# Performance work log

Hardware: AMD Instinct MI355X
Metric: run time of the kernel (lower is better)

## Reference

```python
import jax, jax.numpy as jnp
import numpy as np

B, N, C, H, M, T, L = 2, 4096, 256, 8, 48, 10000, 256
CH = C // H
HID = 512  # mlp_ratio=2


def _ln(x, g, b, eps=1e-5):
    mu = x.mean(-1, keepdims=True)
    var = ((x - mu) ** 2).mean(-1, keepdims=True)
    return (x - mu) * jax.lax.rsqrt(var + eps) * g + b


def setup_inputs() -> dict:
    key = jax.random.key(0)
    ks = iter(jax.random.split(key, 40))
    nrm = lambda shape, s=0.02: jax.random.normal(next(ks), shape, jnp.float32) * s
    return dict(
        feat=jax.random.normal(next(ks), (B, N, C), jnp.float32),
        memory=jax.random.normal(next(ks), (B, L, C), jnp.float32),
        member_idx=jax.random.randint(next(ks), (B, N, M), 0, N),
        cluster_mask=jax.random.randint(next(ks), (B, N, M), 0, 2, jnp.int32),
        pe_idx=jax.random.randint(next(ks), (B, N, M), 0, T),
        global_attn=0,
        pre_table=jax.random.normal(next(ks), (T, 5), jnp.float32),
        Wq=nrm((C, C)), bq=jnp.zeros(C), Wkv=nrm((C, 2 * C)), bkv=jnp.zeros(2 * C),
        blank_k=nrm((C,), 1.0), blank_v=nrm((C,), 1.0),
        Wpe=nrm((5, H)), bpe=jnp.zeros(H),
        Wproj=nrm((C, C)), bproj=jnp.zeros(C),
        g1=jnp.ones(C), be1=jnp.zeros(C), g2=jnp.ones(C), be2=jnp.zeros(C),
        xWq=nrm((C, C)), xbq=jnp.zeros(C), xWk=nrm((C, C)), xbk=jnp.zeros(C),
        xWv=nrm((C, C)), xbv=jnp.zeros(C), xWo=nrm((C, C)), xbo=jnp.zeros(C),
        xg=jnp.ones(C), xbe=jnp.zeros(C),
        W1=nrm((C, HID)), bf1=jnp.zeros(HID), W2=nrm((HID, C)), bf2=jnp.zeros(C),
    )


def _cluster_attn(x, member_idx, cluster_mask, pe_idx, pre_table,
                  Wq, bq, Wkv, bkv, blank_k, blank_v, Wpe, bpe, Wproj, bproj):
    b, n, c = x.shape
    scale = CH ** -0.5
    q = ((x @ Wq + bq) * scale).reshape(b, n, H, CH).transpose(0, 2, 1, 3)  # bhnc
    kv = (x @ Wkv + bkv).reshape(b, n, H, 2, CH)
    k = kv[..., 0, :].transpose(0, 2, 1, 3)  # bhnc
    v = kv[..., 1, :].transpose(0, 2, 1, 3)  # bhnc
    # CLUSTENQK: gather per-token neighborhood keys, dot with q -> b h n m
    gather = jax.vmap(lambda t, idx: t[:, idx, :])  # (h,n,c),(n,m)->(h,n,m,c)
    k_g = gather(k, member_idx)
    attn = jnp.einsum('bhnc,bhnmc->bhnm', q, k_g)
    # positional embedding table lookup
    pe_table = pre_table @ Wpe + bpe                 # T x H
    pos = pe_table[pe_idx].transpose(0, 3, 1, 2)     # b h n m
    attn = attn + pos
    maskf = cluster_mask.astype(attn.dtype)[:, None]  # b 1 n m
    attn = attn + (1.0 - maskf) * -100.0
    blank_attn = jnp.einsum('bhnc,hc->bhn', q, blank_k.reshape(H, CH))[..., None]
    p = jax.nn.softmax(jnp.concatenate([attn, blank_attn], axis=-1), axis=-1)
    pa, pb = p[..., :-1], p[..., -1:]
    # CLUSTENAV: gather values, weighted sum
    v_g = gather(v, member_idx)
    out = jnp.einsum('bhnm,bhnmc->bhnc', pa, v_g)
    out = out + pb * blank_v.reshape(1, H, 1, CH)
    out = out.transpose(0, 2, 1, 3).reshape(b, n, c)
    return out @ Wproj + bproj


def _cross_attn(tgt, memory, xWq, xbq, xWk, xbk, xWv, xbv, xWo, xbo, xg, xbe):
    b, n, c = tgt.shape
    t2 = _ln(tgt, xg, xbe)  # normalize_before=True
    q = (t2 @ xWq + xbq).reshape(b, n, H, CH).transpose(0, 2, 1, 3) * (CH ** -0.5)
    k = (memory @ xWk + xbk).reshape(b, -1, H, CH).transpose(0, 2, 1, 3)
    v = (memory @ xWv + xbv).reshape(b, -1, H, CH).transpose(0, 2, 1, 3)
    p = jax.nn.softmax(jnp.einsum('bhnc,bhlc->bhnl', q, k), axis=-1)
    o = jnp.einsum('bhnl,bhlc->bhnc', p, v).transpose(0, 2, 1, 3).reshape(b, n, c)
    return tgt + (o @ xWo + xbo)


def reference(feat, memory, member_idx, cluster_mask, pe_idx, global_attn, pre_table,
              Wq, bq, Wkv, bkv, blank_k, blank_v, Wpe, bpe, Wproj, bproj,
              g1, be1, g2, be2,
              xWq, xbq, xWk, xbk, xWv, xbv, xWo, xbo, xg, xbe,
              W1, bf1, W2, bf2):
    # global_attn is a static flag; this reference covers the local-cluster path
    assert global_attn == 0
    # local cluster attention with pre-norm residual (drop_path/layer_scale disabled)
    feat = feat + _cluster_attn(_ln(feat, g1, be1), member_idx, cluster_mask, pe_idx,
                                pre_table, Wq, bq, Wkv, bkv, blank_k, blank_v,
                                Wpe, bpe, Wproj, bproj)
    # cross attention to memory (pre-norm, residual inside)
    feat = _cross_attn(feat, memory, xWq, xbq, xWk, xbk, xWv, xbv, xWo, xbo, xg, xbe)
    # MLP block
    h = jax.nn.gelu(_ln(feat, g2, be2) @ W1 + bf1, approximate=False)
    feat = feat + (h @ W2 + bf2)
    return feat
```

## Files before the change

kernel.cpp:

```cpp
#include <hip/hip_runtime.h>
#include <hip/hip_bf16.h>
#include <math.h>

#define BB 2
#define NN 4096
#define CC 256
#define HH 8
#define MM 48
#define TT 10000
#define LL 256
#define CHDIM 32
#define HIDD 512
#define ROWS (BB*NN)

typedef __attribute__((ext_vector_type(8))) short bf16x8;
typedef __attribute__((ext_vector_type(4))) float f32x4;

static __device__ __forceinline__ short f2bf(float x) {
    __hip_bfloat16 h = __float2bfloat16(x);
    return *reinterpret_cast<short*>(&h);
}
static __device__ __forceinline__ float bf2f(short s) {
    unsigned int u = ((unsigned int)(unsigned short)s) << 16;
    union { unsigned int u; float f; } c; c.u = u;
    return c.f;
}

struct WtDesc { const float* src; __hip_bfloat16* dst; int K; int N; int tile0; float scl; };
struct WtArgs { WtDesc d[9]; };

__global__ __launch_bounds__(256) void prep_all_kernel(WtArgs a,
    const float* __restrict__ pre, const float* __restrict__ Wpe,
    const float* __restrict__ bpe, float* __restrict__ pet,
    const float* __restrict__ bq, const float* __restrict__ bkv,
    const float* __restrict__ xbk, const float* __restrict__ xbv,
    const float* __restrict__ xbq, float scale,
    float* __restrict__ bqkv, float* __restrict__ xbkv, float* __restrict__ xbqS,
    const float* __restrict__ memory, __hip_bfloat16* __restrict__ memBf) {
    __shared__ float tile[32][33];
    int bid = blockIdx.x, tid = threadIdx.x;
    if (bid < 768) {
        int mi = 0;
        #pragma unroll
        for (int i = 1; i < 9; ++i) if (bid >= a.d[i].tile0) mi = i;
        WtDesc dsc = a.d[mi];
        int t = bid - dsc.tile0;
        int tiles_n = dsc.N >> 5;
        int k0 = (t / tiles_n) * 32, n0 = (t % tiles_n) * 32;
        int tx = tid & 31, ty = tid >> 5;
        #pragma unroll
        for (int i = 0; i < 32; i += 8)
            tile[ty + i][tx] = dsc.src[(size_t)(k0 + ty + i) * dsc.N + n0 + tx];
        __syncthreads();
        #pragma unroll
        for (int i = 0; i < 32; i += 8)
            dsc.dst[(size_t)(n0 + ty + i) * dsc.K + k0 + tx] = __float2bfloat16(tile[tx][ty + i] * dsc.scl);
        return;
    }
    bid -= 768;
    if (bid < 313) {
        int i = bid * 256 + tid;
        if (i >= TT * HH) return;
        int t = i / HH, h = i % HH;
        float s = bpe[h];
        #pragma unroll
        for (int j = 0; j < 5; ++j) s += pre[t * 5 + j] * Wpe[j * HH + h];
        pet[i] = s;
    } else if (bid < 319) {
        int i = (bid - 313) * 256 + tid;
        if (i < 256) bqkv[i] = bq[i] * scale;
        else if (i < 768) bqkv[i] = bkv[i - 256];
        else if (i < 1024) xbkv[i - 768] = xbk[i - 768];
        else if (i < 1280) xbkv[256 + i - 1024] = xbv[i - 1024];
        else if (i < 1536) xbqS[i - 1280] = xbq[i - 1280] * scale;
    } else {
        int i = (bid - 319) * 256 + tid;
        if (i < 131072) memBf[i] = __float2bfloat16(memory[i]);
    }
}

__global__ __launch_bounds__(256) void ln_kernel(const float* __restrict__ in,
                                                 const float* __restrict__ g,
                                                 const float* __restrict__ b,
                                                 __hip_bfloat16* __restrict__ out) {
    int wave = threadIdx.x >> 6, lane = threadIdx.x & 63;
    int row = blockIdx.x * 4 + wave;
    float4 v = ((const float4*)(in + (size_t)row * CC))[lane];
    float s = (v.x + v.y) + (v.z + v.w);
    #pragma unroll
    for (int off = 32; off; off >>= 1) s += __shfl_xor(s, off, 64);
    float mu = s * (1.0f / 256.0f);
    float dx = v.x - mu, dy = v.y - mu, dz = v.z - mu, dw = v.w - mu;
    float s2 = (dx * dx + dy * dy) + (dz * dz + dw * dw);
    #pragma unroll
    for (int off = 32; off; off >>= 1) s2 += __shfl_xor(s2, off, 64);
    float rs = rsqrtf(s2 * (1.0f / 256.0f) + 1e-5f);
    float4 g4 = ((const float4*)g)[lane];
    float4 b4 = ((const float4*)b)[lane];
    ushort4 o4;
    o4.x = (unsigned short)f2bf(dx * rs * g4.x + b4.x);
    o4.y = (unsigned short)f2bf(dy * rs * g4.y + b4.y);
    o4.z = (unsigned short)f2bf(dz * rs * g4.z + b4.z);
    o4.w = (unsigned short)f2bf(dw * rs * g4.w + b4.w);
    *(ushort4*)((unsigned short*)out + (size_t)row * CC + lane * 4) = o4;
}

#define GBM 128
#define GBN 64
#define GBK 64
#define LDA 72
template<int ACT, int OUTBF>
__device__ __forceinline__ void gemm_body(short* As, short* Bs,
    const __hip_bfloat16* __restrict__ A, const __hip_bfloat16* __restrict__ BT,
    const float* __restrict__ bias, void* __restrict__ outv,
    const float* __restrict__ residual, int N, int K, int row0, int col0) {
    int tid = threadIdx.x;
    int lane = tid & 63, wid = tid >> 6;
    int wr = wid >> 1, wc = wid & 1;
    int lr = lane & 15, lk = lane >> 4;
    f32x4 acc[4][2] = {};
    for (int kt = 0; kt < K; kt += GBK) {
        #pragma unroll
        for (int i = 0; i < 4; ++i) {
            int flat = tid + i * 256;
            int r = flat >> 3, kc = (flat & 7) * 8;
            *(bf16x8*)&As[r * LDA + kc] = *(const bf16x8*)(A + (size_t)(row0 + r) * K + kt + kc);
        }
        #pragma unroll
        for (int i = 0; i < 2; ++i) {
            int flat = tid + i * 256;
            int r = flat >> 3, kc = (flat & 7) * 8;
            *(bf16x8*)&Bs[r * LDA + kc] = *(const bf16x8*)(BT + (size_t)(col0 + r) * K + kt + kc);
        }
        __syncthreads();
        #pragma unroll
        for (int ks = 0; ks < 2; ++ks) {
            bf16x8 bfr[2];
            #pragma unroll
            for (int n = 0; n < 2; ++n)
                bfr[n] = *(const bf16x8*)&Bs[(wc * 32 + n * 16 + lr) * LDA + ks * 32 + lk * 8];
            #pragma unroll
            for (int m = 0; m < 4; ++m) {
                bf16x8 afr = *(const bf16x8*)&As[(wr * 64 + m * 16 + lr) * LDA + ks * 32 + lk * 8];
                #pragma unroll
                for (int n = 0; n < 2; ++n)
                    acc[m][n] = __builtin_amdgcn_mfma_f32_16x16x32_bf16(afr, bfr[n], acc[m][n], 0, 0, 0);
            }
        }
        __syncthreads();
    }
    float bv[2];
    #pragma unroll
    for (int n = 0; n < 2; ++n) bv[n] = bias[col0 + wc * 32 + n * 16 + lr];
    #pragma unroll
    for (int m = 0; m < 4; ++m) {
        #pragma unroll
        for (int n = 0; n < 2; ++n) {
            int col = col0 + wc * 32 + n * 16 + lr;
            #pragma unroll
            for (int r = 0; r < 4; ++r) {
                int row = row0 + wr * 64 + m * 16 + lk * 4 + r;
                float v = acc[m][n][r] + bv[n];
                if (ACT == 1) v = 0.5f * v * (1.0f + erff(v * 0.70710678118654752f));
                size_t oi = (size_t)row * N + col;
                if (residual) v += residual[oi];
                if (OUTBF) ((__hip_bfloat16*)outv)[oi] = __float2bfloat16(v);
                else ((float*)outv)[oi] = v;
            }
        }
    }
}

template<int ACT, int OUTBF>
__global__ __launch_bounds__(256) void mfma_gemm_kernel(
    const __hip_bfloat16* __restrict__ A, const __hip_bfloat16* __restrict__ BT,
    const float* __restrict__ bias, void* __restrict__ outv,
    const float* __restrict__ residual, int M, int N, int K) {
    __shared__ short As[GBM * LDA];
    __shared__ short Bs[GBN * LDA];
    gemm_body<ACT, OUTBF>(As, Bs, A, BT, bias, outv, residual, N, K,
                          blockIdx.y * GBM, blockIdx.x * GBN);
}

struct GemmPair {
    const __hip_bfloat16 *A1, *B1; const float* bias1; void* out1;
    const __hip_bfloat16 *A2, *B2; const float* bias2; void* out2;
};
__global__ __launch_bounds__(256) void dual_gemm_kernel(GemmPair p) {
    __shared__ short As[GBM * LDA];
    __shared__ short Bs[GBN * LDA];
    if (blockIdx.x < 4) {
        gemm_body<0, 1>(As, Bs, p.A1, p.B1, p.bias1, p.out1, nullptr, 256, 256,
                        blockIdx.y * GBM, blockIdx.x * GBN);
    } else {
        int row0 = blockIdx.y * GBM;
        if (row0 >= 512) return;
        gemm_body<0, 1>(As, Bs, p.A2, p.B2, p.bias2, p.out2, nullptr, 512, 256,
                        row0, (blockIdx.x - 4) * GBN);
    }
}

#define KVSTR 520
__global__ __launch_bounds__(512) void cluster_attn_kernel(
    const __hip_bfloat16* __restrict__ qkvh,
    const int* __restrict__ member_idx, const int* __restrict__ cluster_mask,
    const int* __restrict__ pe_idx, const float* __restrict__ pet,
    const float* __restrict__ blank_k, const float* __restrict__ blank_v,
    __hip_bfloat16* __restrict__ outp) {
    const short* qkv = (const short*)qkvh;
    __shared__ short s_kv[48 * KVSTR];
    __shared__ float s_pm[48 * 9];
    __shared__ float s_q[256];
    int tid = threadIdx.x;
    int row = blockIdx.x;
    int b = row >> 12;

    {
        int w = tid >> 6, l = tid & 63;
        #pragma unroll
        for (int r = 0; r < 6; ++r) {
            int m = w + r * 8;
            int im = member_idx[(size_t)row * MM + m];
            bf16x8 v8 = *(const bf16x8*)(qkv + ((size_t)(b * NN + im)) * 768 + 256 + l * 8);
            *(bf16x8*)&s_kv[m * KVSTR + l * 8] = v8;
        }
    }
    if (tid < MM) {
        float mb = cluster_mask[(size_t)row * MM + tid] ? 0.0f : -100.0f;
        int pidx = pe_idx[(size_t)row * MM + tid];
        const float4* pr = (const float4*)(pet + (size_t)pidx * 8);
        float4 p0 = pr[0], p1 = pr[1];
        float* dst = &s_pm[tid * 9];
        dst[0] = p0.x + mb; dst[1] = p0.y + mb; dst[2] = p0.z + mb; dst[3] = p0.w + mb;
        dst[4] = p1.x + mb; dst[5] = p1.y + mb; dst[6] = p1.z + mb; dst[7] = p1.w + mb;
    } else if (tid >= 256) {
        s_q[tid - 256] = bf2f(qkv[(size_t)row * 768 + (tid - 256)]);
    }
    __syncthreads();

    int h = tid >> 6, lane = tid & 63;
    const float* qf = s_q + h * CHDIM;
    float e = 0.0f;
    if (lane < MM) {
        const short* krow = s_kv + lane * KVSTR + h * 64;
        float d = s_pm[lane * 9 + h];
        #pragma unroll
        for (int c8 = 0; c8 < 4; ++c8) {
            bf16x8 kk = *(const bf16x8*)(krow + c8 * 8);
            d += qf[c8 * 8 + 0] * bf2f(kk[0]) + qf[c8 * 8 + 1] * bf2f(kk[1])
               + qf[c8 * 8 + 2] * bf2f(kk[2]) + qf[c8 * 8 + 3] * bf2f(kk[3])
               + qf[c8 * 8 + 4] * bf2f(kk[4]) + qf[c8 * 8 + 5] * bf2f(kk[5])
               + qf[c8 * 8 + 6] * bf2f(kk[6]) + qf[c8 * 8 + 7] * bf2f(kk[7]);
        }
        e = __expf(d);
    } else if (lane == MM) {
        const float* bk = blank_k + h * CHDIM;
        float d = 0.0f;
        #pragma unroll
        for (int c = 0; c < CHDIM; ++c) d += qf[c] * bk[c];
        e = __expf(d);
    }
    float ssum = e;
    #pragma unroll
    for (int off = 32; off; off >>= 1) ssum += __shfl_xor(ssum, off, 64);
    float p = e / ssum;
    float p48 = __shfl(p, MM, 64);

    int mg = lane >> 3, cq = lane & 7;
    float a0 = 0.f, a1 = 0.f, a2 = 0.f, a3 = 0.f;
    #pragma unroll
    for (int it = 0; it < 6; ++it) {
        int m = it * 8 + mg;
        float pm = __shfl(p, m, 64);
        const short* vp = s_kv + m * KVSTR + h * 64 + 32 + cq * 4;
        ushort4 vv = *(const ushort4*)vp;
        a0 += pm * bf2f(vv.x); a1 += pm * bf2f(vv.y);
        a2 += pm * bf2f(vv.z); a3 += pm * bf2f(vv.w);
    }
    #pragma unroll
    for (int off = 8; off < 64; off <<= 1) {
        a0 += __shfl_xor(a0, off, 64);
        a1 += __shfl_xor(a1, off, 64);
        a2 += __shfl_xor(a2, off, 64);
        a3 += __shfl_xor(a3, off, 64);
    }
    if (lane < 8) {
        const float* bvp = blank_v + h * CHDIM + cq * 4;
        a0 += p48 * bvp[0]; a1 += p48 * bvp[1]; a2 += p48 * bvp[2]; a3 += p48 * bvp[3];
        ushort4 o4;
        o4.x = (unsigned short)f2bf(a0); o4.y = (unsigned short)f2bf(a1);
        o4.z = (unsigned short)f2bf(a2); o4.w = (unsigned short)f2bf(a3);
        *(ushort4*)((unsigned short*)outp + (size_t)row * CC + h * CHDIM + cq * 4) = o4;
    }
}

#define KSLD 40
#define PVLD 264
__global__ __launch_bounds__(256) void cross_attn_kernel(
    const __hip_bfloat16* __restrict__ xq,
    const __hip_bfloat16* __restrict__ xkvh,
    __hip_bfloat16* __restrict__ o) {
    const short* xkv = (const short*)xkvh;
    extern __shared__ short lds[];
    short* Ks = lds;
    short* Vt = lds + 256 * KSLD;
    short* Ps = Vt + 32 * PVLD;
    int tid = threadIdx.x, lane = tid & 63, w = tid >> 6;
    int tile = blockIdx.x, h = blockIdx.y, b = blockIdx.z;
    int lr = lane & 15, g = lane >> 4;

    #pragma unroll
    for (int p = 0; p < 8; ++p) {
        int l = p * 32 + (tid >> 3);
        int c4 = (tid & 7) * 4;
        const short* kvrow = xkv + ((size_t)(b * LL + l)) * 512 + h * CHDIM;
        ushort4 kk = *(const ushort4*)(kvrow + c4);
        *(ushort4*)&Ks[l * KSLD + c4] = kk;
        ushort4 vv = *(const ushort4*)(kvrow + 256 + c4);
        Vt[(c4 + 0) * PVLD + l] = vv.x;
        Vt[(c4 + 1) * PVLD + l] = vv.y;
        Vt[(c4 + 2) * PVLD + l] = vv.z;
        Vt[(c4 + 3) * PVLD + l] = vv.w;
    }
    __syncthreads();

    int qrow = b * NN + tile * 64 + w * 16 + lr;
    bf16x8 afr = *(const bf16x8*)(xq + (size_t)qrow * CC + h * CHDIM + g * 8);
    f32x4 s[16];
    #pragma unroll
    for (int t = 0; t < 16; ++t) {
        bf16x8 kb = *(const bf16x8*)&Ks[(t * 16 + lr) * KSLD + g * 8];
        s[t] = __builtin_amdgcn_mfma_f32_16x16x32_bf16(afr, kb, (f32x4){0.f,0.f,0.f,0.f}, 0, 0, 0);
    }
    float rs[4] = {0.f, 0.f, 0.f, 0.f};
    #pragma unroll
    for (int t = 0; t < 16; ++t)
        #pragma unroll
        for (int r = 0; r < 4; ++r) { float e = __expf(s[t][r]); s[t][r] = e; rs[r] += e; }
    #pragma unroll
    for (int off = 1; off < 16; off <<= 1)
        #pragma unroll
        for (int r = 0; r < 4; ++r) rs[r] += __shfl_xor(rs[r], off, 64);
    short* Pw = Ps + w * 16 * PVLD;
    #pragma unroll
    for (int t = 0; t < 16; ++t)
        #pragma unroll
        for (int r = 0; r < 4; ++r)
            Pw[(g * 4 + r) * PVLD + t * 16 + lr] = f2bf(s[t][r]);
    f32x4 oacc[2] = {};
    #pragma unroll
    for (int kc = 0; kc < 8; ++kc) {
        bf16x8 pa = *(const bf16x8*)&Pw[lr * PVLD + kc * 32 + g * 8];
        #pragma unroll
        for (int n = 0; n < 2; ++n) {
            bf16x8 vb = *(const bf16x8*)&Vt[(n * 16 + lr) * PVLD + kc * 32 + g * 8];
            oacc[n] = __builtin_amdgcn_mfma_f32_16x16x32_bf16(pa, vb, oacc[n], 0, 0, 0);
        }
    }
    float inv[4];
    #pragma unroll
    for (int r = 0; r < 4; ++r) inv[r] = 1.0f / rs[r];
    #pragma unroll
    for (int n = 0; n < 2; ++n)
        #pragma unroll
        for (int r = 0; r < 4; ++r) {
            int orow = b * NN + tile * 64 + w * 16 + g * 4 + r;
            o[(size_t)orow * CC + h * CHDIM + n * 16 + lr] = __float2bfloat16(oacc[n][r] * inv[r]);
        }
}

extern "C" void kernel_launch(void* const* d_in, const int* in_sizes, int n_in,
                              void* d_out, int out_size, void* d_ws, size_t ws_size,
                              hipStream_t stream) {
    const float* feat        = (const float*)d_in[0];
    const float* memory      = (const float*)d_in[1];
    const int*   member_idx  = (const int*)d_in[2];
    const int*   cluster_mask= (const int*)d_in[3];
    const int*   pe_idx      = (const int*)d_in[4];
    const float* pre_table   = (const float*)d_in[6];
    const float* Wq    = (const float*)d_in[7];
    const float* bq    = (const float*)d_in[8];
    const float* Wkv   = (const float*)d_in[9];
    const float* bkv   = (const float*)d_in[10];
    const float* blank_k = (const float*)d_in[11];
    const float* blank_v = (const float*)d_in[12];
    const float* Wpe   = (const float*)d_in[13];
    const float* bpe   = (const float*)d_in[14];
    const float* Wproj = (const float*)d_in[15];
    const float* bproj = (const float*)d_in[16];
    const float* g1    = (const float*)d_in[17];
    const float* be1   = (const float*)d_in[18];
    const float* g2    = (const float*)d_in[19];
    const float* be2   = (const float*)d_in[20];
    const float* xWq   = (const float*)d_in[21];
    const float* xbq   = (const float*)d_in[22];
    const float* xWk   = (const float*)d_in[23];
    const float* xbk   = (const float*)d_in[24];
    const float* xWv   = (const float*)d_in[25];
    const float* xbv   = (const float*)d_in[26];
    const float* xWo   = (const float*)d_in[27];
    const float* xbo   = (const float*)d_in[28];
    const float* xg    = (const float*)d_in[29];
    const float* xbe   = (const float*)d_in[30];
    const float* W1    = (const float*)d_in[31];
    const float* bf1   = (const float*)d_in[32];
    const float* W2    = (const float*)d_in[33];
    const float* bf2   = (const float*)d_in[34];
    float* out = (float*)d_out;
    float* ws  = (float*)d_ws;

    __hip_bfloat16* qkvBf = (__hip_bfloat16*)ws;
    __hip_bfloat16* xqBf  = (__hip_bfloat16*)ws;
    __hip_bfloat16* xkvBf = (__hip_bfloat16*)(ws + 3145728);
    __hip_bfloat16* hBf   = (__hip_bfloat16*)(ws + 3276800);
    float* feat1F = ws + 5373952;
    __hip_bfloat16* aBf   = (__hip_bfloat16*)(ws + 7471104);
    __hip_bfloat16* oBf   = (__hip_bfloat16*)(ws + 8519680);
    __hip_bfloat16* WqkvT = (__hip_bfloat16*)(ws + 9568256);
    __hip_bfloat16* WprojT= (__hip_bfloat16*)(ws + 9666560);
    __hip_bfloat16* xWqT  = (__hip_bfloat16*)(ws + 9699328);
    __hip_bfloat16* xWoT  = (__hip_bfloat16*)(ws + 9732096);
    __hip_bfloat16* xWkvT = (__hip_bfloat16*)(ws + 9764864);
    __hip_bfloat16* W1T   = (__hip_bfloat16*)(ws + 9830400);
    __hip_bfloat16* W2T   = (__hip_bfloat16*)(ws + 9895936);
    __hip_bfloat16* memBf = (__hip_bfloat16*)(ws + 9961472);
    float* pet   = ws + 10027008;
    float* bqkv  = ws + 10107008;
    float* xbkv  = ws + 10107776;
    float* xbqS  = ws + 10108288;

    const float scale = 0.17677669529663689f;

    WtArgs wa;
    wa.d[0] = { Wq,    WqkvT,          256, 256, 0,   scale };
    wa.d[1] = { Wkv,   WqkvT + 65536,  256, 512, 64,  1.0f };
    wa.d[2] = { Wproj, WprojT,         256, 256, 192, 1.0f };
    wa.d[3] = { xWq,   xWqT,           256, 256, 256, scale };
    wa.d[4] = { xWk,   xWkvT,          256, 256, 320, 1.0f };
    wa.d[5] = { xWv,   xWkvT + 65536,  256, 256, 384, 1.0f };
    wa.d[6] = { xWo,   xWoT,           256, 256, 448, 1.0f };
    wa.d[7] = { W1,    W1T,            256, 512, 512, 1.0f };
    wa.d[8] = { W2,    W2T,            512, 256, 640, 1.0f };
    prep_all_kernel<<<768 + 831, 256, 0, stream>>>(wa, pre_table, Wpe, bpe, pet,
                                                   bq, bkv, xbk, xbv, xbq, scale,
                                                   bqkv, xbkv, xbqS, memory, memBf);

    ln_kernel<<<ROWS / 4, 256, 0, stream>>>(feat, g1, be1, aBf);
    mfma_gemm_kernel<0,1><<<dim3(12, 64), 256, 0, stream>>>(aBf, WqkvT, bqkv, qkvBf, nullptr, ROWS, 768, 256);
    cluster_attn_kernel<<<ROWS, 512, 0, stream>>>(qkvBf, member_idx, cluster_mask, pe_idx, pet, blank_k, blank_v, oBf);
    mfma_gemm_kernel<0,0><<<dim3(4, 64), 256, 0, stream>>>(oBf, WprojT, bproj, feat1F, feat, ROWS, 256, 256);
    ln_kernel<<<ROWS / 4, 256, 0, stream>>>(feat1F, xg, xbe, aBf);
    {
        GemmPair gp;
        gp.A1 = aBf;   gp.B1 = xWqT;  gp.bias1 = xbqS; gp.out1 = xqBf;
        gp.A2 = memBf; gp.B2 = xWkvT; gp.bias2 = xbkv; gp.out2 = xkvBf;
        dual_gemm_kernel<<<dim3(12, 64), 256, 0, stream>>>(gp);
    }
    {
        size_t xlds = (256 * KSLD + 32 * PVLD + 4 * 16 * PVLD) * sizeof(short);
        cross_attn_kernel<<<dim3(NN / 64, HH, BB), 256, xlds, stream>>>(xqBf, xkvBf, oBf);
    }
    mfma_gemm_kernel<0,0><<<dim3(4, 64), 256, 0, stream>>>(oBf, xWoT, xbo, out, feat1F, ROWS, 256, 256);
    ln_kernel<<<ROWS / 4, 256, 0, stream>>>(out, g2, be2, aBf);
    mfma_gemm_kernel<1,1><<<dim3(8, 64), 256, 0, stream>>>(aBf, W1T, bf1, hBf, nullptr, ROWS, HIDD, 256);
    mfma_gemm_kernel<0,0><<<dim3(4, 64), 256, 0, stream>>>(hBf, W2T, bf2, out, out, ROWS, 256, HIDD);
}
```

Before: 162.2 us.

## Store cluster-attention K/V in FP8 and reorder block-to-row mapping

The QKV GEMM now writes Q as bf16 and K/V as FP8 e4m3 into a separate buffer. The cluster attention kernel gathers 8-byte FP8 rows instead of 16-byte bf16 rows and decodes them with packed fp8-to-f32 conversions, halving the bytes moved by the random neighbour gather. Blocks are also remapped so consecutive block IDs stride across rows, which changes how gather locality spreads over the device. The cost is lower K/V precision (e4m3 on unscaled activations), which risks accuracy error.

```diff
diff --git a/kernel.cpp b/kernel.cpp
--- a/kernel.cpp
+++ b/kernel.cpp
@@ -1,5 +1,6 @@
 #include <hip/hip_runtime.h>
 #include <hip/hip_bf16.h>
+#include <hip/hip_fp8.h>
 #include <math.h>
 
 #define BB 2
@@ -15,6 +16,7 @@
 
 typedef __attribute__((ext_vector_type(8))) short bf16x8;
 typedef __attribute__((ext_vector_type(4))) float f32x4;
+typedef __attribute__((ext_vector_type(2))) float f32x2;
 
 static __device__ __forceinline__ short f2bf(float x) {
     __hip_bfloat16 h = __float2bfloat16(x);
@@ -109,11 +111,12 @@
 #define GBN 64
 #define GBK 64
 #define LDA 72
-template<int ACT, int OUTBF>
+template<int ACT, int OUTM>
 __device__ __forceinline__ void gemm_body(short* As, short* Bs,
     const __hip_bfloat16* __restrict__ A, const __hip_bfloat16* __restrict__ BT,
     const float* __restrict__ bias, void* __restrict__ outv,
-    const float* __restrict__ residual, int N, int K, int row0, int col0) {
+    const float* __restrict__ residual, int N, int K, int row0, int col0,
+    void* __restrict__ outv2) {
     int tid = threadIdx.x;
     int lane = tid & 63, wid = tid >> 6;
     int wr = wid >> 1, wc = wid & 1;
@@ -162,24 +165,34 @@
                 int row = row0 + wr * 64 + m * 16 + lk * 4 + r;
                 float v = acc[m][n][r] + bv[n];
                 if (ACT == 1) v = 0.5f * v * (1.0f + erff(v * 0.70710678118654752f));
-                size_t oi = (size_t)row * N + col;
-                if (residual) v += residual[oi];
-                if (OUTBF) ((__hip_bfloat16*)outv)[oi] = __float2bfloat16(v);
-                else ((float*)outv)[oi] = v;
+                if (OUTM == 2) {
+                    if (col < 256) {
+                        ((__hip_bfloat16*)outv)[(size_t)row * 256 + col] = __float2bfloat16(v);
+                    } else {
+                        __hip_fp8_e4m3 f8(v);
+                        ((unsigned char*)outv2)[(size_t)row * 512 + (col - 256)] = f8.__x;
+                    }
+                } else {
+                    size_t oi = (size_t)row * N + col;
+                    if (residual) v += residual[oi];
+                    if (OUTM == 1) ((__hip_bfloat16*)outv)[oi] = __float2bfloat16(v);
+                    else ((float*)outv)[oi] = v;
+                }
             }
         }
     }
 }
 
-template<int ACT, int OUTBF>
+template<int ACT, int OUTM>
 __global__ __launch_bounds__(256) void mfma_gemm_kernel(
     const __hip_bfloat16* __restrict__ A, const __hip_bfloat16* __restrict__ BT,
     const float* __restrict__ bias, void* __restrict__ outv,
-    const float* __restrict__ residual, int M, int N, int K) {
+    const float* __restrict__ residual, int M, int N, int K,
+    void* __restrict__ outv2) {
     __shared__ short As[GBM * LDA];
     __shared__ short Bs[GBN * LDA];
-    gemm_body<ACT, OUTBF>(As, Bs, A, BT, bias, outv, residual, N, K,
-                          blockIdx.y * GBM, blockIdx.x * GBN);
+    gemm_body<ACT, OUTM>(As, Bs, A, BT, bias, outv, residual, N, K,
+                         blockIdx.y * GBM, blockIdx.x * GBN, outv2);
 }
 
 struct GemmPair {
@@ -191,28 +204,30 @@
     __shared__ short Bs[GBN * LDA];
     if (blockIdx.x < 4) {
         gemm_body<0, 1>(As, Bs, p.A1, p.B1, p.bias1, p.out1, nullptr, 256, 256,
-                        blockIdx.y * GBM, blockIdx.x * GBN);
+                        blockIdx.y * GBM, blockIdx.x * GBN, nullptr);
     } else {
         int row0 = blockIdx.y * GBM;
         if (row0 >= 512) return;
         gemm_body<0, 1>(As, Bs, p.A2, p.B2, p.bias2, p.out2, nullptr, 512, 256,
-                        row0, (blockIdx.x - 4) * GBN);
-    }
-}
-
-#define KVSTR 520
+                        row0, (blockIdx.x - 4) * GBN, nullptr);
+    }
+}
+
+#define KVSTR8 528
 __global__ __launch_bounds__(512) void cluster_attn_kernel(
-    const __hip_bfloat16* __restrict__ qkvh,
+    const __hip_bfloat16* __restrict__ qh,
+    const unsigned char* __restrict__ kv8,
     const int* __restrict__ member_idx, const int* __restrict__ cluster_mask,
     const int* __restrict__ pe_idx, const float* __restrict__ pet,
     const float* __restrict__ blank_k, const float* __restrict__ blank_v,
     __hip_bfloat16* __restrict__ outp) {
-    const short* qkv = (const short*)qkvh;
-    __shared__ short s_kv[48 * KVSTR];
+    const short* qg = (const short*)qh;
+    __shared__ unsigned char s_kv[48 * KVSTR8];
     __shared__ float s_pm[48 * 9];
     __shared__ float s_q[256];
     int tid = threadIdx.x;
-    int row = blockIdx.x;
+    int bid = blockIdx.x;
+    int row = ((bid & 7) << 10) | (bid >> 3);
     int b = row >> 12;
 
     {
@@ -221,8 +236,8 @@
         for (int r = 0; r < 6; ++r) {
             int m = w + r * 8;
             int im = member_idx[(size_t)row * MM + m];
-            bf16x8 v8 = *(const bf16x8*)(qkv + ((size_t)(b * NN + im)) * 768 + 256 + l * 8);
-            *(bf16x8*)&s_kv[m * KVSTR + l * 8] = v8;
+            uint2 v8 = *(const uint2*)(kv8 + ((size_t)(b * NN + im)) * 512 + l * 8);
+            *(uint2*)&s_kv[m * KVSTR8 + l * 8] = v8;
         }
     }
     if (tid < MM) {
@@ -234,7 +249,7 @@
         dst[0] = p0.x + mb; dst[1] = p0.y + mb; dst[2] = p0.z + mb; dst[3] = p0.w + mb;
         dst[4] = p1.x + mb; dst[5] = p1.y + mb; dst[6] = p1.z + mb; dst[7] = p1.w + mb;
     } else if (tid >= 256) {
-        s_q[tid - 256] = bf2f(qkv[(size_t)row * 768 + (tid - 256)]);
+        s_q[tid - 256] = bf2f(qg[(size_t)row * CC + (tid - 256)]);
     }
     __syncthreads();
 
@@ -242,15 +257,15 @@
     const float* qf = s_q + h * CHDIM;
     float e = 0.0f;
     if (lane < MM) {
-        const short* krow = s_kv + lane * KVSTR + h * 64;
+        const unsigned int* kp = (const unsigned int*)(s_kv + lane * KVSTR8 + h * 64);
         float d = s_pm[lane * 9 + h];
         #pragma unroll
-        for (int c8 = 0; c8 < 4; ++c8) {
-            bf16x8 kk = *(const bf16x8*)(krow + c8 * 8);
-            d += qf[c8 * 8 + 0] * bf2f(kk[0]) + qf[c8 * 8 + 1] * bf2f(kk[1])
-               + qf[c8 * 8 + 2] * bf2f(kk[2]) + qf[c8 * 8 + 3] * bf2f(kk[3])
-               + qf[c8 * 8 + 4] * bf2f(kk[4]) + qf[c8 * 8 + 5] * bf2f(kk[5])
-               + qf[c8 * 8 + 6] * bf2f(kk[6]) + qf[c8 * 8 + 7] * bf2f(kk[7]);
+        for (int u = 0; u < 8; ++u) {
+            unsigned int kw = kp[u];
+            f32x2 k01 = __builtin_amdgcn_cvt_pk_f32_fp8(kw, 0);
+            f32x2 k23 = __builtin_amdgcn_cvt_pk_f32_fp8(kw, 1);
+            d += qf[u * 4 + 0] * k01.x + qf[u * 4 + 1] * k01.y
+               + qf[u * 4 + 2] * k23.x + qf[u * 4 + 3] * k23.y;
         }
         e = __expf(d);
     } else if (lane == MM) {
@@ -272,10 +287,11 @@
     for (int it = 0; it < 6; ++it) {
         int m = it * 8 + mg;
         float pm = __shfl(p, m, 64);
-        const short* vp = s_kv + m * KVSTR + h * 64 + 32 + cq * 4;
-        ushort4 vv = *(const ushort4*)vp;
-        a0 += pm * bf2f(vv.x); a1 += pm * bf2f(vv.y);
-        a2 += pm * bf2f(vv.z); a3 += pm * bf2f(vv.w);
+        unsigned int vw = *(const unsigned int*)(s_kv + m * KVSTR8 + h * 64 + 32 + cq * 4);
+        f32x2 v01 = __builtin_amdgcn_cvt_pk_f32_fp8(vw, 0);
+        f32x2 v23 = __builtin_amdgcn_cvt_pk_f32_fp8(vw, 1);
+        a0 += pm * v01.x; a1 += pm * v01.y;
+        a2 += pm * v23.x; a3 += pm * v23.y;
     }
     #pragma unroll
     for (int off = 8; off < 64; off <<= 1) {
@@ -409,25 +425,26 @@
     float* out = (float*)d_out;
     float* ws  = (float*)d_ws;
 
-    __hip_bfloat16* qkvBf = (__hip_bfloat16*)ws;
+    __hip_bfloat16* qBf   = (__hip_bfloat16*)ws;
     __hip_bfloat16* xqBf  = (__hip_bfloat16*)ws;
-    __hip_bfloat16* xkvBf = (__hip_bfloat16*)(ws + 3145728);
-    __hip_bfloat16* hBf   = (__hip_bfloat16*)(ws + 3276800);
-    float* feat1F = ws + 5373952;
-    __hip_bfloat16* aBf   = (__hip_bfloat16*)(ws + 7471104);
-    __hip_bfloat16* oBf   = (__hip_bfloat16*)(ws + 8519680);
-    __hip_bfloat16* WqkvT = (__hip_bfloat16*)(ws + 9568256);
-    __hip_bfloat16* WprojT= (__hip_bfloat16*)(ws + 9666560);
-    __hip_bfloat16* xWqT  = (__hip_bfloat16*)(ws + 9699328);
-    __hip_bfloat16* xWoT  = (__hip_bfloat16*)(ws + 9732096);
-    __hip_bfloat16* xWkvT = (__hip_bfloat16*)(ws + 9764864);
-    __hip_bfloat16* W1T   = (__hip_bfloat16*)(ws + 9830400);
-    __hip_bfloat16* W2T   = (__hip_bfloat16*)(ws + 9895936);
-    __hip_bfloat16* memBf = (__hip_bfloat16*)(ws + 9961472);
-    float* pet   = ws + 10027008;
-    float* bqkv  = ws + 10107008;
-    float* xbkv  = ws + 10107776;
-    float* xbqS  = ws + 10108288;
+    unsigned char*  kv8   = (unsigned char*)(ws + 1048576);
+    __hip_bfloat16* xkvBf = (__hip_bfloat16*)(ws + 2097152);
+    __hip_bfloat16* hBf   = (__hip_bfloat16*)(ws + 2228224);
+    float* feat1F = ws + 4325376;
+    __hip_bfloat16* aBf   = (__hip_bfloat16*)(ws + 6422528);
+    __hip_bfloat16* oBf   = (__hip_bfloat16*)(ws + 7471104);
+    __hip_bfloat16* WqkvT = (__hip_bfloat16*)(ws + 8519680);
+    __hip_bfloat16* WprojT= (__hip_bfloat16*)(ws + 8617984);
+    __hip_bfloat16* xWqT  = (__hip_bfloat16*)(ws + 8650752);
+    __hip_bfloat16* xWoT  = (__hip_bfloat16*)(ws + 8683520);
+    __hip_bfloat16* xWkvT = (__hip_bfloat16*)(ws + 8716288);
+    __hip_bfloat16* W1T   = (__hip_bfloat16*)(ws + 8781824);
+    __hip_bfloat16* W2T   = (__hip_bfloat16*)(ws + 8847360);
+    __hip_bfloat16* memBf = (__hip_bfloat16*)(ws + 8912896);
+    float* pet   = ws + 8978432;
+    float* bqkv  = ws + 9058432;
+    float* xbkv  = ws + 9059200;
+    float* xbqS  = ws + 9059712;
 
     const float scale = 0.17677669529663689f;
 
@@ -446,9 +463,9 @@
                                                    bqkv, xbkv, xbqS, memory, memBf);
 
     ln_kernel<<<ROWS / 4, 256, 0, stream>>>(feat, g1, be1, aBf);
-    mfma_gemm_kernel<0,1><<<dim3(12, 64), 256, 0, stream>>>(aBf, WqkvT, bqkv, qkvBf, nullptr, ROWS, 768, 256);
-    cluster_attn_kernel<<<ROWS, 512, 0, stream>>>(qkvBf, member_idx, cluster_mask, pe_idx, pet, blank_k, blank_v, oBf);
-    mfma_gemm_kernel<0,0><<<dim3(4, 64), 256, 0, stream>>>(oBf, WprojT, bproj, feat1F, feat, ROWS, 256, 256);
+    mfma_gemm_kernel<0,2><<<dim3(12, 64), 256, 0, stream>>>(aBf, WqkvT, bqkv, qBf, nullptr, ROWS, 768, 256, kv8);
+    cluster_attn_kernel<<<ROWS, 512, 0, stream>>>(qBf, kv8, member_idx, cluster_mask, pe_idx, pet, blank_k, blank_v, oBf);
+    mfma_gemm_kernel<0,0><<<dim3(4, 64), 256, 0, stream>>>(oBf, WprojT, bproj, feat1F, feat, ROWS, 256, 256, nullptr);
     ln_kernel<<<ROWS / 4, 256, 0, stream>>>(feat1F, xg, xbe, aBf);
     {
         GemmPair gp;
@@ -460,8 +477,8 @@
         size_t xlds = (256 * KSLD + 32 * PVLD + 4 * 16 * PVLD) * sizeof(short);
         cross_attn_kernel<<<dim3(NN / 64, HH, BB), 256, xlds, stream>>>(xqBf, xkvBf, oBf);
     }
-    mfma_gemm_kernel<0,0><<<dim3(4, 64), 256, 0, stream>>>(oBf, xWoT, xbo, out, feat1F, ROWS, 256, 256);
+    mfma_gemm_kernel<0,0><<<dim3(4, 64), 256, 0, stream>>>(oBf, xWoT, xbo, out, feat1F, ROWS, 256, 256, nullptr);
     ln_kernel<<<ROWS / 4, 256, 0, stream>>>(out, g2, be2, aBf);
-    mfma_gemm_kernel<1,1><<<dim3(8, 64), 256, 0, stream>>>(aBf, W1T, bf1, hBf, nullptr, ROWS, HIDD, 256);
-    mfma_gemm_kernel<0,0><<<dim3(4, 64), 256, 0, stream>>>(hBf, W2T, bf2, out, out, ROWS, 256, HIDD);
-}
+    mfma_gemm_kernel<1,1><<<dim3(8, 64), 256, 0, stream>>>(aBf, W1T, bf1, hBf, nullptr, ROWS, HIDD, 256, nullptr);
+    mfma_gemm_kernel<0,0><<<dim3(4, 64), 256, 0, stream>>>(hBf, W2T, bf2, out, out, ROWS, 256, HIDD, nullptr);
+}
```

New measurement: 148.6 us. 8.4% less time.
